# Kernel optimization log

Hardware: AMD Instinct MI355X
Metric: run time of the kernel (lower is better)

Reference implementation:

```python
import jax, jax.numpy as jnp
import numpy as np

B, N, F_IN, D = 32768, 4, 512, 64  # N fixed to 4 by the max_pool(4,1)+reshape


def setup_inputs() -> dict:
    key = jax.random.key(0)
    k1, k2, k3, k4 = jax.random.split(key, 4)
    scale = 1.0 / np.sqrt(F_IN)
    return {
        "drug": jax.random.normal(k1, (B, N, F_IN), dtype=jnp.float32),
        "Wk": jax.random.normal(k2, (F_IN, D), dtype=jnp.float32) * scale,
        "Wq": jax.random.normal(k3, (F_IN, D), dtype=jnp.float32) * scale,
        "Wv": jax.random.normal(k4, (F_IN, D), dtype=jnp.float32) * scale,
    }


def reference(drug, Wk, Wq, Wv):
    # projections: torch nn.Linear(bias=False) -> x @ W  (W stored as [in, out] here)
    k = jnp.einsum("bnf,fd->bnd", drug, Wk)
    q = jnp.einsum("bnf,fd->bnd", drug, Wq)
    v = jnp.einsum("bnf,fd->bnd", drug, Wv)
    # score = bmm(K, Q^T); NOTE: no 1/sqrt(d) scaling, matching the source
    score = jnp.einsum("bnd,bmd->bnm", k, q)  # [B, N, N]
    attn = jax.nn.softmax(score, axis=2)
    out = jnp.einsum("bnm,bmd->bnd", attn, v)  # [B, N, D]
    # max_pool2d kernel (4,1), stride (4,1) over N=4 -> max over axis 1, then reshape [B, D]
    return jnp.max(out, axis=1)
```

## Files before the change

kernel.cpp:

```cpp
#include <hip/hip_runtime.h>
#include <hip/hip_fp16.h>

#define BTOT   32768
#define FIN    512
#define NCOLS  192
#define KSTEPS 16
#define NTILES 12
#define WH_ELEMS (KSTEPS * NTILES * 64 * 8)
#define CHUNK_HALVES (NTILES * 64 * 8)

using half8   = __attribute__((ext_vector_type(8))) _Float16;
using floatx4 = __attribute__((ext_vector_type(4))) float;

__global__ void convert_w_kernel(const float* __restrict__ Wk,
                                 const float* __restrict__ Wq,
                                 const float* __restrict__ Wv,
                                 _Float16* __restrict__ Wh) {
    int idx = blockIdx.x * blockDim.x + threadIdx.x;
    if (idx >= WH_ELEMS) return;
    int j    = idx & 7;
    int lane = (idx >> 3) & 63;
    int t    = (idx >> 9) % NTILES;
    int kk   = idx / CHUNK_HALVES;
    int k = kk * 32 + (lane >> 4) * 8 + j;
    int n = t * 16 + (lane & 15);
    const float* src = (n < 64) ? Wk : (n < 128) ? Wq : Wv;
    Wh[idx] = (_Float16)src[k * 64 + (n & 63)];
}

__global__ __launch_bounds__(256, 4) void attn_fused_kernel(
        const float* __restrict__ drug,
        const _Float16* __restrict__ Wh,
        float* __restrict__ out)
{
    const int tid  = threadIdx.x;
    const int wave = tid >> 6;
    const int lane = tid & 63;
    const int quad = lane >> 4;
    const int l15  = lane & 15;

    const int row = blockIdx.x * 64 + wave * 16 + l15;
    const float* arow = drug + (size_t)row * FIN + quad * 8;
    const half8* bbase = (const half8*)(Wh + lane * 8);

    floatx4 acc[NTILES];
#pragma unroll
    for (int t = 0; t < NTILES; ++t) acc[t] = (floatx4){0.f, 0.f, 0.f, 0.f};

    for (int kk = 0; kk < KSTEPS; ++kk) {
        const float4* ap = (const float4*)(arow + kk * 32);
        float4 a0 = ap[0];
        float4 a1 = ap[1];

        const half8* bp = bbase + kk * (CHUNK_HALVES / 8);

        half8 afrag;
        afrag[0] = (_Float16)a0.x; afrag[1] = (_Float16)a0.y;
        afrag[2] = (_Float16)a0.z; afrag[3] = (_Float16)a0.w;
        afrag[4] = (_Float16)a1.x; afrag[5] = (_Float16)a1.y;
        afrag[6] = (_Float16)a1.z; afrag[7] = (_Float16)a1.w;

#pragma unroll
        for (int t = 0; t < NTILES; ++t) {
            half8 bfrag = bp[t * 64];
            acc[t] = __builtin_amdgcn_mfma_f32_16x16x32_f16(afrag, bfrag, acc[t], 0, 0, 0);
        }
    }

    float p[4][4];
#pragma unroll
    for (int n = 0; n < 4; ++n)
#pragma unroll
        for (int m = 0; m < 4; ++m) {
            float s = 0.f;
#pragma unroll
            for (int t = 0; t < 4; ++t) s += acc[t][n] * acc[4 + t][m];
            p[n][m] = s;
        }

#pragma unroll
    for (int mask = 1; mask < 16; mask <<= 1) {
#pragma unroll
        for (int n = 0; n < 4; ++n)
#pragma unroll
            for (int m = 0; m < 4; ++m)
                p[n][m] += __shfl_xor(p[n][m], mask, 64);
    }

    float res[4] = {-INFINITY, -INFINITY, -INFINITY, -INFINITY};
#pragma unroll
    for (int n = 0; n < 4; ++n) {
        float mx = fmaxf(fmaxf(p[n][0], p[n][1]), fmaxf(p[n][2], p[n][3]));
        float e0 = __expf(p[n][0] - mx);
        float e1 = __expf(p[n][1] - mx);
        float e2 = __expf(p[n][2] - mx);
        float e3 = __expf(p[n][3] - mx);
        float inv = 1.f / (e0 + e1 + e2 + e3);
#pragma unroll
        for (int t = 0; t < 4; ++t) {
            float o = (e0 * acc[8 + t][0] + e1 * acc[8 + t][1] +
                       e2 * acc[8 + t][2] + e3 * acc[8 + t][3]) * inv;
            res[t] = fmaxf(res[t], o);
        }
    }

    const int b = blockIdx.x * 16 + wave * 4 + quad;
#pragma unroll
    for (int t = 0; t < 4; ++t)
        out[b * 64 + t * 16 + l15] = res[t];
}

extern "C" void kernel_launch(void* const* d_in, const int* in_sizes, int n_in,
                              void* d_out, int out_size, void* d_ws, size_t ws_size,
                              hipStream_t stream) {
    const float* drug = (const float*)d_in[0];
    const float* Wk   = (const float*)d_in[1];
    const float* Wq   = (const float*)d_in[2];
    const float* Wv   = (const float*)d_in[3];
    float* out = (float*)d_out;
    _Float16* Wh = (_Float16*)d_ws;

    convert_w_kernel<<<(WH_ELEMS + 255) / 256, 256, 0, stream>>>(Wk, Wq, Wv, Wh);
    attn_fused_kernel<<<BTOT / 16, 256, 0, stream>>>(drug, Wh, out);
}
```

Measured before the change: 412.9 us.

## Stage fp16 weight chunks in LDS via global_load_lds shared across waves

Each block now copies two k-steps of the packed fp16 weight tiles into shared memory with direct global-to-LDS loads. All four waves then read their B fragments from LDS instead of each wave fetching the same weights from global memory or L2. This cuts redundant weight traffic by the number of waves per block. The cost is two block-wide barriers per phase and a single, non-double-buffered LDS stage, so load latency is not overlapped with MFMA work. The min-blocks occupancy hint in the launch bounds is also dropped.

Result: faster. 367.0 us (-11.1%).

```diff
diff --git a/kernel.cpp b/kernel.cpp
--- a/kernel.cpp
+++ b/kernel.cpp
@@ -8,9 +8,16 @@
 #define NTILES 12
 #define WH_ELEMS (KSTEPS * NTILES * 64 * 8)
 #define CHUNK_HALVES (NTILES * 64 * 8)
+#define CHUNK_BYTES  (CHUNK_HALVES * 2)
+#define PHASES 8
 
 using half8   = __attribute__((ext_vector_type(8))) _Float16;
 using floatx4 = __attribute__((ext_vector_type(4))) float;
+
+#define GLOAD_LDS16(gp, lp)                                                  \
+    __builtin_amdgcn_global_load_lds(                                        \
+        (const __attribute__((address_space(1))) void*)(gp),                 \
+        (__attribute__((address_space(3))) void*)(lp), 16, 0, 0)
 
 __global__ void convert_w_kernel(const float* __restrict__ Wk,
                                  const float* __restrict__ Wq,
@@ -28,11 +35,13 @@
     Wh[idx] = (_Float16)src[k * 64 + (n & 63)];
 }
 
-__global__ __launch_bounds__(256, 4) void attn_fused_kernel(
+__global__ __launch_bounds__(256) void attn_fused_kernel(
         const float* __restrict__ drug,
         const _Float16* __restrict__ Wh,
         float* __restrict__ out)
 {
+    __shared__ __align__(16) char lds[2 * CHUNK_BYTES];
+
     const int tid  = threadIdx.x;
     const int wave = tid >> 6;
     const int lane = tid & 63;
@@ -41,29 +50,47 @@
 
     const int row = blockIdx.x * 64 + wave * 16 + l15;
     const float* arow = drug + (size_t)row * FIN + quad * 8;
-    const half8* bbase = (const half8*)(Wh + lane * 8);
+    const char* gW = (const char*)Wh;
 
     floatx4 acc[NTILES];
 #pragma unroll
     for (int t = 0; t < NTILES; ++t) acc[t] = (floatx4){0.f, 0.f, 0.f, 0.f};
 
-    for (int kk = 0; kk < KSTEPS; ++kk) {
-        const float4* ap = (const float4*)(arow + kk * 32);
-        float4 a0 = ap[0];
-        float4 a1 = ap[1];
+    for (int ph = 0; ph < PHASES; ++ph) {
+        __syncthreads();
 
-        const half8* bp = bbase + kk * (CHUNK_HALVES / 8);
+        const size_t goff = (size_t)ph * 2 * CHUNK_BYTES;
+#pragma unroll
+        for (int i = 0; i < 6; ++i) {
+            const int off = i * 4096 + wave * 1024;
+            GLOAD_LDS16(gW + goff + off + lane * 16, lds + off);
+        }
 
-        half8 afrag;
-        afrag[0] = (_Float16)a0.x; afrag[1] = (_Float16)a0.y;
-        afrag[2] = (_Float16)a0.z; afrag[3] = (_Float16)a0.w;
-        afrag[4] = (_Float16)a1.x; afrag[5] = (_Float16)a1.y;
-        afrag[6] = (_Float16)a1.z; afrag[7] = (_Float16)a1.w;
+        const float4* ap0 = (const float4*)(arow + (2 * ph) * 32);
+        const float4* ap1 = (const float4*)(arow + (2 * ph + 1) * 32);
+        float4 a00 = ap0[0], a01 = ap0[1];
+        float4 a10 = ap1[0], a11 = ap1[1];
+
+        half8 afrag[2];
+        afrag[0][0] = (_Float16)a00.x; afrag[0][1] = (_Float16)a00.y;
+        afrag[0][2] = (_Float16)a00.z; afrag[0][3] = (_Float16)a00.w;
+        afrag[0][4] = (_Float16)a01.x; afrag[0][5] = (_Float16)a01.y;
+        afrag[0][6] = (_Float16)a01.z; afrag[0][7] = (_Float16)a01.w;
+        afrag[1][0] = (_Float16)a10.x; afrag[1][1] = (_Float16)a10.y;
+        afrag[1][2] = (_Float16)a10.z; afrag[1][3] = (_Float16)a10.w;
+        afrag[1][4] = (_Float16)a11.x; afrag[1][5] = (_Float16)a11.y;
+        afrag[1][6] = (_Float16)a11.z; afrag[1][7] = (_Float16)a11.w;
+
+        __syncthreads();
 
 #pragma unroll
-        for (int t = 0; t < NTILES; ++t) {
-            half8 bfrag = bp[t * 64];
-            acc[t] = __builtin_amdgcn_mfma_f32_16x16x32_f16(afrag, bfrag, acc[t], 0, 0, 0);
+        for (int s = 0; s < 2; ++s) {
+            const _Float16* lh = (const _Float16*)(lds + s * CHUNK_BYTES);
+#pragma unroll
+            for (int t = 0; t < NTILES; ++t) {
+                half8 bfrag = *((const half8*)(lh + (t * 64 + lane) * 8));
+                acc[t] = __builtin_amdgcn_mfma_f32_16x16x32_f16(afrag[s], bfrag, acc[t], 0, 0, 0);
+            }
         }
     }
 
```
